# Performance work log

Hardware: AMD Instinct MI355X
Metric: run time of the kernel (lower is better)

The kernel has to match this reference:

```python
import jax, jax.numpy as jnp
import numpy as np

B, N, HIST, PRED, KHOP, H = 64, 1085, 24, 24, 3, 64
FX, FM = 1, 11
F = FX + FM  # node feature dim fed to gnn (12)
E = 17360


def setup_inputs() -> dict:
    key = jax.random.key(0)
    ks = jax.random.split(key, 13)
    s = 0.1
    return {
        "x_hist": jax.random.normal(ks[0], (B, HIST, N, FX), jnp.float32),
        "enc_misc": jax.random.normal(ks[1], (B, HIST, N, FM), jnp.float32),
        "dec": jax.random.normal(ks[2], (B, PRED, N, FM), jnp.float32),
        "We": jax.random.normal(ks[3], (2 * F, F), jnp.float32) * s,
        "be": jnp.zeros((F,), jnp.float32),
        "Wx": jax.random.normal(ks[4], (KHOP, 2 * F, 3 * H), jnp.float32) * s,
        "Wh": jax.random.normal(ks[5], (KHOP, H, 3 * H), jnp.float32) * s,
        "bx": jnp.zeros((KHOP, 3 * H), jnp.float32),
        "bh": jnp.zeros((KHOP, 3 * H), jnp.float32),
        "fc_w": jax.random.normal(ks[6], (KHOP * H, FX), jnp.float32) * s,
        "fc_b": jnp.zeros((FX,), jnp.float32),
        "src": jax.random.randint(ks[7], (E,), 0, N, jnp.int32),
        "dst": jax.random.randint(ks[8], (E,), 0, N, jnp.int32),
    }


def reference(x_hist, enc_misc, dec, We, be, Wx, Wh, bx, bh, fc_w, fc_b, src, dst):
    features = jnp.concatenate([enc_misc, dec], axis=1)  # (B, HIST+PRED, N, FM)

    def gnn(x):  # x: (B, N, F) -> (B, N, F); edge MLP + scatter-sum + residual
        m = jax.nn.relu(jnp.concatenate([x[:, src], x[:, dst]], -1) @ We + be)  # (B,E,F)
        return x + jnp.zeros_like(x).at[:, dst].add(m)

    def gru(x, h, k):  # x: (B*N, 2F), h: (B*N, H)
        g = x @ Wx[k] + bx[k]
        gh = h @ Wh[k] + bh[k]
        r = jax.nn.sigmoid(g[:, :H] + gh[:, :H])
        z = jax.nn.sigmoid(g[:, H:2 * H] + gh[:, H:2 * H])
        n = jnp.tanh(g[:, 2 * H:] + r * gh[:, 2 * H:])
        return (1.0 - z) * n + z * h

    def run_step(hn, xn):  # xn: (B, N, F)
        xg = xn
        new = list(hn)
        for k in range(KHOP):
            xg = gnn(xg)
            x_gru = jnp.concatenate([xg, xn], -1).reshape(B * N, 2 * F)
            new[k] = gru(x_gru, new[k], k)
        return tuple(new)

    h0 = tuple(jnp.zeros((B * N, H), x_hist.dtype) for _ in range(KHOP))

    def hist_step(hn, inp):
        xp, ft = inp  # (B,N,FX), (B,N,FM)
        return run_step(hn, jnp.concatenate([xp, ft], -1)), None

    hist_xs = (jnp.swapaxes(x_hist[:, :HIST - 1], 0, 1),
               jnp.swapaxes(features[:, 1:HIST], 0, 1))
    hn, _ = jax.lax.scan(hist_step, h0, hist_xs)

    def pred_step(carry, ft):
        hn, x = carry
        hn = run_step(hn, jnp.concatenate([x, ft], -1))
        hn_all = jnp.concatenate([h.reshape(B, N, H) for h in hn], -1)  # (B,N,KHOP*H)
        x_new = hn_all @ fc_w + fc_b  # (B, N, FX)
        return (hn, x_new), x_new

    _, ys = jax.lax.scan(pred_step, (hn, x_hist[:, -1]),
                         jnp.swapaxes(features[:, HIST:], 0, 1))
    return jnp.swapaxes(ys, 0, 1)  # (B, PRED, N, FX)
```

## Files before the change

### kernel.cpp

```cpp
#include <hip/hip_runtime.h>

#define NB 64
#define NNODE 1085
#define HIST 24
#define PRED 24
#define KHOP 3
#define HDIM 64
#define FXD 1
#define FMD 11
#define FD 12
#define NE 17360
#define NROWS (NB*NNODE)
#define CHUNK 136

typedef float v4 __attribute__((ext_vector_type(4)));

__device__ __forceinline__ float sigm(float x){ return 1.0f/(1.0f + __expf(-x)); }
__device__ __forceinline__ float tanh_f(float x){ return 1.0f - 2.0f/(__expf(2.0f*x)+1.0f); }

__global__ void csr_count_k(const int* __restrict__ dst, int* __restrict__ deg)
{
    int e = blockIdx.x*256 + threadIdx.x;
    if (e < NE) atomicAdd(&deg[dst[e]], 1);
}

__global__ __launch_bounds__(1024) void csr_scan_k(const int* __restrict__ deg,
                                                   int* __restrict__ offs, int* __restrict__ curs)
{
    __shared__ int s[2][2048];
    int t = threadIdx.x;
    for (int i=t;i<2048;i+=1024) s[0][i] = (i<NNODE) ? deg[i] : 0;
    __syncthreads();
    int cur = 0;
    for (int d=1; d<2048; d<<=1){
        for (int i=t;i<2048;i+=1024){
            int v = s[cur][i];
            if (i>=d) v += s[cur][i-d];
            s[cur^1][i] = v;
        }
        __syncthreads();
        cur ^= 1;
    }
    for (int i=t;i<=NNODE;i+=1024){
        int v = (i==0) ? 0 : s[cur][i-1];
        offs[i] = v;
        if (i<NNODE) curs[i] = v;
    }
}

__global__ void csr_fill_k(const int* __restrict__ dst, int* __restrict__ curs,
                           int* __restrict__ elist)
{
    int e = blockIdx.x*256 + threadIdx.x;
    if (e < NE){
        int d = dst[e];
        int p = atomicAdd(&curs[d], 1);
        elist[p] = e;
    }
}

__global__ void build_hist_k(const float* __restrict__ x_hist, const float* __restrict__ enc_misc,
                             int t0, int T, float* __restrict__ xn_all)
{
    int idx = blockIdx.x*256 + threadIdx.x;
    if (idx >= T*NROWS) return;
    int ti = idx / NROWS, row = idx - ti*NROWS;
    int b = row / NNODE, n = row - b*NNODE;
    int t = t0 + ti;
    float v[12];
    v[0] = x_hist[((long)b*HIST + t)*NNODE + n];
    const float* fp = enc_misc + (((long)b*HIST + (t+1))*NNODE + n)*FMD;
    #pragma unroll
    for (int i=0;i<FMD;i++) v[1+i] = fp[i];
    v4* xp = (v4*)(xn_all + ((long)ti*NROWS + row)*FD);
    #pragma unroll
    for (int q=0;q<3;q++){
        v4 tq; tq[0]=v[4*q]; tq[1]=v[4*q+1]; tq[2]=v[4*q+2]; tq[3]=v[4*q+3];
        xp[q]=tq;
    }
}

__global__ void build_xn_k(const float* __restrict__ xsrc, long xs_bs, long xs_off,
                           const float* __restrict__ feat, long f_bs, long f_off,
                           float* __restrict__ xn)
{
    int row = blockIdx.x*256 + threadIdx.x;
    if (row >= NROWS) return;
    int b = row / NNODE, n = row - b*NNODE;
    float v[12];
    v[0] = xsrc[(long)b*xs_bs + xs_off + n];
    const float* fp = feat + (long)b*f_bs + f_off + (long)n*FMD;
    #pragma unroll
    for (int i=0;i<FMD;i++) v[1+i] = fp[i];
    v4* xp = (v4*)(xn + (long)row*FD);
    #pragma unroll
    for (int q=0;q<3;q++){
        v4 tq; tq[0]=v[4*q]; tq[1]=v[4*q+1]; tq[2]=v[4*q+2]; tq[3]=v[4*q+3];
        xp[q]=tq;
    }
}

__global__ __launch_bounds__(256) void gnn_gather_k(const float* __restrict__ xin,
    const float* __restrict__ We, const float* __restrict__ be,
    const int* __restrict__ src, const int* __restrict__ dst,
    const int* __restrict__ elist, const int* __restrict__ offs,
    float* __restrict__ xout)
{
    __shared__ __align__(16) float x_s[NNODE*FD];
    __shared__ __align__(16) float acc_s[CHUNK*FD];
    __shared__ __align__(16) float w_s[288];
    __shared__ float be_s[12];
    const int t = threadIdx.x;
    const int b = blockIdx.x >> 3, c = blockIdx.x & 7;
    const long ti = blockIdx.y;
    const int n0 = c*CHUNK, n1 = min(NNODE, n0+CHUNK);
    const float* x = xin + ti*NROWS*FD;

    const v4* xg4 = (const v4*)(x + (long)b*NNODE*FD);
    for (int i=t; i<NNODE*FD/4; i+=256) ((v4*)x_s)[i] = xg4[i];
    for (int i=t; i<288; i+=256) w_s[i]=We[i];
    if (t<12) be_s[t]=be[t];
    for (int i=t; i<(n1-n0)*FD; i+=256) acc_s[i]=0.f;
    __syncthreads();

    const int e_beg = offs[n0], e_end = offs[n1];
    const int total = e_end - e_beg;
    const int L = (total + 255) >> 8;
    const int my_beg = e_beg + t*L;
    const int my_end = min(my_beg + L, e_end);

    float accr[12];
    float part[12];
    int cur = -1;

    for (int idx=my_beg; idx<my_end; ++idx){
        int e = elist[idx];
        int sN = src[e], dN = dst[e];
        if (dN != cur){
            if (cur >= 0){
                float* ab = &acc_s[(cur-n0)*FD];
                #pragma unroll
                for (int f=0;f<12;f++) atomicAdd(&ab[f], accr[f]);
            }
            cur = dN;
            #pragma unroll
            for (int f=0;f<12;f++){ accr[f]=0.f; part[f]=be_s[f]; }
            const v4* xdv = (const v4*)&x_s[dN*FD];
            #pragma unroll
            for (int q=0;q<3;q++){
                v4 cc = xdv[q];
                #pragma unroll
                for (int j=0;j<4;j++){
                    float xv = cc[j];
                    int i = (12 + 4*q + j)*12;
                    v4 w0=*(const v4*)&w_s[i];
                    v4 w1=*(const v4*)&w_s[i+4];
                    v4 w2=*(const v4*)&w_s[i+8];
                    #pragma unroll
                    for (int jj=0;jj<4;jj++){
                        part[jj]   += xv*w0[jj];
                        part[4+jj] += xv*w1[jj];
                        part[8+jj] += xv*w2[jj];
                    }
                }
            }
        }
        float m[12];
        #pragma unroll
        for (int f=0;f<12;f++) m[f]=part[f];
        const v4* xsv = (const v4*)&x_s[sN*FD];
        #pragma unroll
        for (int q=0;q<3;q++){
            v4 a = xsv[q];
            #pragma unroll
            for (int j=0;j<4;j++){
                float xv = a[j];
                int i = (4*q + j)*12;
                v4 w0=*(const v4*)&w_s[i];
                v4 w1=*(const v4*)&w_s[i+4];
                v4 w2=*(const v4*)&w_s[i+8];
                #pragma unroll
                for (int jj=0;jj<4;jj++){
                    m[jj]   += xv*w0[jj];
                    m[4+jj] += xv*w1[jj];
                    m[8+jj] += xv*w2[jj];
                }
            }
        }
        #pragma unroll
        for (int f=0;f<12;f++) accr[f] += fmaxf(m[f], 0.f);
    }
    if (cur >= 0){
        float* ab = &acc_s[(cur-n0)*FD];
        #pragma unroll
        for (int f=0;f<12;f++) atomicAdd(&ab[f], accr[f]);
    }
    __syncthreads();

    const int cnt4 = (n1-n0)*FD/4;
    const v4* xs4 = (const v4*)&x_s[n0*FD];
    const v4* ac4 = (const v4*)acc_s;
    v4* ob4 = (v4*)(xout + ti*NROWS*FD + ((long)b*NNODE + n0)*FD);
    for (int i=t; i<cnt4; i+=256) ob4[i] = xs4[i] + ac4[i];
}

#define KC 44
__global__ __launch_bounds__(256) void gru3_k(
    const float* __restrict__ xg_base, long k_stride,
    const float* __restrict__ xn,
    float* __restrict__ h_base,
    const float* __restrict__ Wx, const float* __restrict__ Wh,
    const float* __restrict__ bx, const float* __restrict__ bh)
{
    const int k = blockIdx.y;
    const float* xg  = xg_base + (long)k*k_stride;
    float*       h   = h_base + (size_t)k*NROWS*HDIM;
    const float* wx  = Wx + (size_t)k*24*192;
    const float* wh  = Wh + (size_t)k*64*192;
    const float* bxk = bx + k*192;
    const float* bhk = bh + k*192;

    __shared__ __align__(16) float A_s[KC][64];
    __shared__ __align__(16) float W_s[KC][192];
    const int tid = threadIdx.x;
    const int tx = tid & 15, ty = tid >> 4;
    const long row0 = (long)blockIdx.x * 64;

    const v4* xg4 = (const v4*)(xg + row0*FD);
    const v4* xn4 = (const v4*)(xn + row0*FD);
    const v4* h4  = (const v4*)(h  + row0*HDIM);
    const v4* wx4 = (const v4*)wx;
    const v4* wh4 = (const v4*)wh;

    float acc_r[16], acc_z[16], acc_gn[16], acc_ghn[16];
    #pragma unroll
    for (int i=0;i<16;i++){ acc_r[i]=0.f; acc_z[i]=0.f; acc_gn[i]=0.f; acc_ghn[i]=0.f; }

    for (int i=tid; i<KC*48; i+=256){
        int kk = i/48, q = i - kk*48;
        v4 w = (kk<24) ? wx4[kk*48+q] : wh4[(kk-24)*48+q];
        *(v4*)&W_s[kk][q*4] = w;
    }
    for (int i=tid; i<192; i+=256){
        int r = i/3, q = i - r*3;
        v4 v = xg4[r*3+q];
        #pragma unroll
        for (int j=0;j<4;j++) A_s[4*q+j][r] = v[j];
    }
    for (int i=tid; i<192; i+=256){
        int r = i/3, q = i - r*3;
        v4 v = xn4[r*3+q];
        #pragma unroll
        for (int j=0;j<4;j++) A_s[12+4*q+j][r] = v[j];
    }
    for (int i=tid; i<320; i+=256){
        int r = i/5, q = i - r*5;
        v4 v = h4[r*16+q];
        #pragma unroll
        for (int j=0;j<4;j++) A_s[24+4*q+j][r] = v[j];
    }
    __syncthreads();
    #pragma unroll 4
    for (int kk=0;kk<24;kk++){
        v4 av=*(const v4*)&A_s[kk][ty*4];
        v4 wr=*(const v4*)&W_s[kk][tx*4];
        v4 wz=*(const v4*)&W_s[kk][64+tx*4];
        v4 wn=*(const v4*)&W_s[kk][128+tx*4];
        #pragma unroll
        for (int dr=0;dr<4;dr++)
            #pragma unroll
            for (int dc=0;dc<4;dc++){
                acc_r[dr*4+dc]+=av[dr]*wr[dc];
                acc_z[dr*4+dc]+=av[dr]*wz[dc];
                acc_gn[dr*4+dc]+=av[dr]*wn[dc];
            }
    }
    #pragma unroll 4
    for (int kk=24;kk<44;kk++){
        v4 av=*(const v4*)&A_s[kk][ty*4];
        v4 wr=*(const v4*)&W_s[kk][tx*4];
        v4 wz=*(const v4*)&W_s[kk][64+tx*4];
        v4 wn=*(const v4*)&W_s[kk][128+tx*4];
        #pragma unroll
        for (int dr=0;dr<4;dr++)
            #pragma unroll
            for (int dc=0;dc<4;dc++){
                acc_r[dr*4+dc]+=av[dr]*wr[dc];
                acc_z[dr*4+dc]+=av[dr]*wz[dc];
                acc_ghn[dr*4+dc]+=av[dr]*wn[dc];
            }
    }
    __syncthreads();
    for (int i=tid; i<KC*48; i+=256){
        int kk = i/48, q = i - kk*48;
        *(v4*)&W_s[kk][q*4] = wh4[(20+kk)*48+q];
    }
    for (int i=tid; i<704; i+=256){
        int r = i/11, q = i - r*11;
        v4 v = h4[r*16+5+q];
        #pragma unroll
        for (int j=0;j<4;j++) A_s[4*q+j][r] = v[j];
    }
    __syncthreads();
    #pragma unroll 4
    for (int kk=0;kk<44;kk++){
        v4 av=*(const v4*)&A_s[kk][ty*4];
        v4 wr=*(const v4*)&W_s[kk][tx*4];
        v4 wz=*(const v4*)&W_s[kk][64+tx*4];
        v4 wn=*(const v4*)&W_s[kk][128+tx*4];
        #pragma unroll
        for (int dr=0;dr<4;dr++)
            #pragma unroll
            for (int dc=0;dc<4;dc++){
                acc_r[dr*4+dc]+=av[dr]*wr[dc];
                acc_z[dr*4+dc]+=av[dr]*wz[dc];
                acc_ghn[dr*4+dc]+=av[dr]*wn[dc];
            }
    }

    v4 bxr=*(const v4*)&bxk[tx*4],     bhr=*(const v4*)&bhk[tx*4];
    v4 bxz=*(const v4*)&bxk[64+tx*4],  bhz=*(const v4*)&bhk[64+tx*4];
    v4 bxn=*(const v4*)&bxk[128+tx*4], bhn=*(const v4*)&bhk[128+tx*4];
    #pragma unroll
    for (int dr=0;dr<4;dr++){
        long row = row0 + ty*4 + dr;
        v4 hold = *(const v4*)&h[row*HDIM + tx*4];
        v4 hnew;
        #pragma unroll
        for (int dc=0;dc<4;dc++){
            float rr = sigm(acc_r[dr*4+dc] + bxr[dc] + bhr[dc]);
            float zz = sigm(acc_z[dr*4+dc] + bxz[dc] + bhz[dc]);
            float nn = tanh_f(acc_gn[dr*4+dc] + bxn[dc] + rr*(acc_ghn[dr*4+dc] + bhn[dc]));
            hnew[dc] = (1.0f-zz)*nn + zz*hold[dc];
        }
        *(v4*)&h[row*HDIM + tx*4] = hnew;
    }
}

__global__ void fc_k(const float* __restrict__ h, const float* __restrict__ fc_w,
                     const float* __restrict__ fc_b, float* __restrict__ x_cur,
                     float* __restrict__ out, int p)
{
    int row = blockIdx.x*256+threadIdx.x;
    if (row>=NROWS) return;
    float acc = fc_b[0];
    #pragma unroll
    for (int k=0;k<3;k++){
        const float* hb = h + (long)k*NROWS*HDIM + (long)row*HDIM;
        const float* wb = fc_w + k*HDIM;
        #pragma unroll
        for (int q=0;q<16;q++){
            v4 hv=*(const v4*)&hb[q*4];
            v4 wv=*(const v4*)&wb[q*4];
            acc += hv[0]*wv[0]+hv[1]*wv[1]+hv[2]*wv[2]+hv[3]*wv[3];
        }
    }
    x_cur[row]=acc;
    int b=row/NNODE, n=row-b*NNODE;
    out[((long)b*PRED + p)*NNODE + n] = acc;
}

extern "C" void kernel_launch(void* const* d_in, const int* in_sizes, int n_in,
                              void* d_out, int out_size, void* d_ws, size_t ws_size,
                              hipStream_t stream)
{
    const float* x_hist   = (const float*)d_in[0];
    const float* enc_misc = (const float*)d_in[1];
    const float* dec      = (const float*)d_in[2];
    const float* We       = (const float*)d_in[3];
    const float* be       = (const float*)d_in[4];
    const float* Wx       = (const float*)d_in[5];
    const float* Wh       = (const float*)d_in[6];
    const float* bx       = (const float*)d_in[7];
    const float* bh       = (const float*)d_in[8];
    const float* fc_w     = (const float*)d_in[9];
    const float* fc_b     = (const float*)d_in[10];
    const int*   src      = (const int*)d_in[11];
    const int*   dst      = (const int*)d_in[12];
    float* out = (float*)d_out;

    const size_t SZ_T = (size_t)NROWS*FD;
    size_t fixed_f = (size_t)3*NROWS*HDIM + NROWS + 32*1024;
    size_t avail_f = ws_size/4;
    long tc = 1;
    if (avail_f > fixed_f + 4*SZ_T)
        tc = (long)((avail_f - fixed_f) / (4*SZ_T));
    if (tc > HIST-1) tc = HIST-1;
    if (tc < 1) tc = 1;
    const long T_CHUNK = tc;

    float* h      = (float*)d_ws;
    float* x_cur  = h + (size_t)3*NROWS*HDIM;
    int*   deg    = (int*)(x_cur + NROWS);
    int*   offs   = deg + NNODE;
    int*   curs   = offs + NNODE + 1;
    int*   elist  = curs + NNODE;
    float* xn_all = (float*)(elist + NE) + 16;
    xn_all = (float*)(((size_t)xn_all + 63) & ~(size_t)63);
    float* xg_all = xn_all + T_CHUNK*SZ_T;
    const long K_STRIDE = T_CHUNK*SZ_T;

    hipMemsetAsync(h, 0, (size_t)3*NROWS*HDIM*sizeof(float), stream);
    hipMemsetAsync(deg, 0, NNODE*sizeof(int), stream);

    const int gE = (NE+255)/256;
    csr_count_k<<<gE,256,0,stream>>>(dst, deg);
    csr_scan_k<<<1,1024,0,stream>>>(deg, offs, curs);
    csr_fill_k<<<gE,256,0,stream>>>(dst, curs, elist);

    const int gRow = (NROWS+255)/256;

    for (int t0 = 0; t0 < HIST-1; t0 += (int)T_CHUNK){
        int T = min((int)T_CHUNK, HIST-1-t0);
        build_hist_k<<<(T*NROWS+255)/256,256,0,stream>>>(x_hist, enc_misc, t0, T, xn_all);
        dim3 gG(NB*8, T);
        gnn_gather_k<<<gG,256,0,stream>>>(xn_all,            We,be,src,dst,elist,offs, xg_all);
        gnn_gather_k<<<gG,256,0,stream>>>(xg_all,            We,be,src,dst,elist,offs, xg_all+K_STRIDE);
        gnn_gather_k<<<gG,256,0,stream>>>(xg_all+K_STRIDE,   We,be,src,dst,elist,offs, xg_all+2*K_STRIDE);
        for (int ti=0; ti<T; ti++){
            dim3 gU(NROWS/64, 3);
            gru3_k<<<gU,256,0,stream>>>(xg_all + ti*SZ_T, K_STRIDE,
                                        xn_all + ti*SZ_T, h, Wx, Wh, bx, bh);
        }
    }

    for (int p=0;p<PRED;p++){
        if (p==0)
            build_xn_k<<<gRow,256,0,stream>>>(x_hist,(long)HIST*NNODE,(long)(HIST-1)*NNODE,
                                              dec,(long)PRED*NNODE*FMD,(long)p*NNODE*FMD, xn_all);
        else
            build_xn_k<<<gRow,256,0,stream>>>(x_cur,(long)NNODE,0L,
                                              dec,(long)PRED*NNODE*FMD,(long)p*NNODE*FMD, xn_all);
        dim3 gG(NB*8, 1);
        gnn_gather_k<<<gG,256,0,stream>>>(xn_all,          We,be,src,dst,elist,offs, xg_all);
        gnn_gather_k<<<gG,256,0,stream>>>(xg_all,          We,be,src,dst,elist,offs, xg_all+K_STRIDE);
        gnn_gather_k<<<gG,256,0,stream>>>(xg_all+K_STRIDE, We,be,src,dst,elist,offs, xg_all+2*K_STRIDE);
        dim3 gU(NROWS/64, 3);
        gru3_k<<<gU,256,0,stream>>>(xg_all, K_STRIDE, xn_all, h, Wx, Wh, bx, bh);
        fc_k<<<gRow,256,0,stream>>>(h, fc_w, fc_b, x_cur, out, p);
    }
}
```

Baseline: 12.02 ms.

## Switch to node-major batch-interleaved layout with wave-per-node-range GNN gather

Node feature tensors are stored node-major with the batch index innermost, so each lane of a 64-wide wave handles one batch element of the same node. The GNN gather no longer stages a whole batch graph in LDS. Each wave walks a precomputed, edge-balanced range of destination nodes and reads source features straight from global memory, coalesced across the batch, with no LDS atomics. The CSR stores source indices directly, the GRU blocks load the now-contiguous per-node tiles without a transpose, and the hidden state becomes node-major. This trades LDS reuse of node features for global/L2 gathers and removes the shared-memory occupancy limit and the atomic reductions.

```diff
diff --git a/kernel.cpp b/kernel.cpp
--- a/kernel.cpp
+++ b/kernel.cpp
@@ -11,7 +11,8 @@
 #define FD 12
 #define NE 17360
 #define NROWS (NB*NNODE)
-#define CHUNK 136
+#define WPAR 1024
+
 
 typedef float v4 __attribute__((ext_vector_type(4)));
 
@@ -48,160 +49,116 @@
     }
 }
 
-__global__ void csr_fill_k(const int* __restrict__ dst, int* __restrict__ curs,
-                           int* __restrict__ elist)
+__global__ void csr_fill_k(const int* __restrict__ dst, const int* __restrict__ src,
+                           int* __restrict__ curs, int* __restrict__ esrc)
 {
     int e = blockIdx.x*256 + threadIdx.x;
     if (e < NE){
         int d = dst[e];
         int p = atomicAdd(&curs[d], 1);
-        elist[p] = e;
-    }
+        esrc[p] = src[e];
+    }
+}
+
+__global__ void csr_part_k(const int* __restrict__ offs, int* __restrict__ wpart)
+{
+    int w = blockIdx.x*256 + threadIdx.x;
+    if (w > WPAR) return;
+    if (w == 0)    { wpart[0] = 0;        return; }
+    if (w == WPAR) { wpart[WPAR] = NNODE; return; }
+    int target = (int)(((long)w * NE) / WPAR);
+    int lo = 0, hi = NNODE;
+    while (lo < hi){ int mid = (lo+hi)>>1; if (offs[mid] >= target) hi = mid; else lo = mid+1; }
+    wpart[w] = lo;
 }
 
 __global__ void build_hist_k(const float* __restrict__ x_hist, const float* __restrict__ enc_misc,
                              int t0, int T, float* __restrict__ xn_all)
 {
+    long idx = (long)blockIdx.x*256 + threadIdx.x;
+    if (idx >= (long)T*NROWS) return;
+    int b = (int)(idx & 63);
+    long nn = idx >> 6;
+    int ti = (int)(nn / NNODE);
+    int n  = (int)(nn - (long)ti*NNODE);
+    int t  = t0 + ti;
+    float* xp = xn_all + (long)ti*NROWS*FD + (long)n*FD*64 + b;
+    xp[0] = x_hist[((long)b*HIST + t)*NNODE + n];
+    const float* fp = enc_misc + (((long)b*HIST + (t+1))*NNODE + n)*FMD;
+    #pragma unroll
+    for (int i=0;i<FMD;i++) xp[(1+i)*64] = fp[i];
+}
+
+__global__ void build_xn_k(const float* __restrict__ xsrc, int from_xcur,
+                           const float* __restrict__ dec, int p,
+                           float* __restrict__ xn)
+{
     int idx = blockIdx.x*256 + threadIdx.x;
-    if (idx >= T*NROWS) return;
-    int ti = idx / NROWS, row = idx - ti*NROWS;
-    int b = row / NNODE, n = row - b*NNODE;
-    int t = t0 + ti;
-    float v[12];
-    v[0] = x_hist[((long)b*HIST + t)*NNODE + n];
-    const float* fp = enc_misc + (((long)b*HIST + (t+1))*NNODE + n)*FMD;
-    #pragma unroll
-    for (int i=0;i<FMD;i++) v[1+i] = fp[i];
-    v4* xp = (v4*)(xn_all + ((long)ti*NROWS + row)*FD);
-    #pragma unroll
-    for (int q=0;q<3;q++){
-        v4 tq; tq[0]=v[4*q]; tq[1]=v[4*q+1]; tq[2]=v[4*q+2]; tq[3]=v[4*q+3];
-        xp[q]=tq;
-    }
-}
-
-__global__ void build_xn_k(const float* __restrict__ xsrc, long xs_bs, long xs_off,
-                           const float* __restrict__ feat, long f_bs, long f_off,
-                           float* __restrict__ xn)
-{
-    int row = blockIdx.x*256 + threadIdx.x;
-    if (row >= NROWS) return;
-    int b = row / NNODE, n = row - b*NNODE;
-    float v[12];
-    v[0] = xsrc[(long)b*xs_bs + xs_off + n];
-    const float* fp = feat + (long)b*f_bs + f_off + (long)n*FMD;
-    #pragma unroll
-    for (int i=0;i<FMD;i++) v[1+i] = fp[i];
-    v4* xp = (v4*)(xn + (long)row*FD);
-    #pragma unroll
-    for (int q=0;q<3;q++){
-        v4 tq; tq[0]=v[4*q]; tq[1]=v[4*q+1]; tq[2]=v[4*q+2]; tq[3]=v[4*q+3];
-        xp[q]=tq;
-    }
+    if (idx >= NROWS) return;
+    int b = idx & 63, n = idx >> 6;
+    float v0 = from_xcur ? xsrc[idx]
+                         : xsrc[((long)b*HIST + (HIST-1))*NNODE + n];
+    float* xp = xn + (long)n*FD*64 + b;
+    xp[0] = v0;
+    const float* fp = dec + (((long)b*PRED + p)*NNODE + n)*FMD;
+    #pragma unroll
+    for (int i=0;i<FMD;i++) xp[(1+i)*64] = fp[i];
 }
 
 __global__ __launch_bounds__(256) void gnn_gather_k(const float* __restrict__ xin,
     const float* __restrict__ We, const float* __restrict__ be,
-    const int* __restrict__ src, const int* __restrict__ dst,
-    const int* __restrict__ elist, const int* __restrict__ offs,
-    float* __restrict__ xout)
-{
-    __shared__ __align__(16) float x_s[NNODE*FD];
-    __shared__ __align__(16) float acc_s[CHUNK*FD];
-    __shared__ __align__(16) float w_s[288];
+    const int* __restrict__ esrc, const int* __restrict__ offs,
+    const int* __restrict__ wpart, float* __restrict__ xout)
+{
+    __shared__ float w_s[288];
     __shared__ float be_s[12];
-    const int t = threadIdx.x;
-    const int b = blockIdx.x >> 3, c = blockIdx.x & 7;
-    const long ti = blockIdx.y;
-    const int n0 = c*CHUNK, n1 = min(NNODE, n0+CHUNK);
-    const float* x = xin + ti*NROWS*FD;
-
-    const v4* xg4 = (const v4*)(x + (long)b*NNODE*FD);
-    for (int i=t; i<NNODE*FD/4; i+=256) ((v4*)x_s)[i] = xg4[i];
-    for (int i=t; i<288; i+=256) w_s[i]=We[i];
-    if (t<12) be_s[t]=be[t];
-    for (int i=t; i<(n1-n0)*FD; i+=256) acc_s[i]=0.f;
-    __syncthreads();
-
-    const int e_beg = offs[n0], e_end = offs[n1];
-    const int total = e_end - e_beg;
-    const int L = (total + 255) >> 8;
-    const int my_beg = e_beg + t*L;
-    const int my_end = min(my_beg + L, e_end);
-
-    float accr[12];
-    float part[12];
-    int cur = -1;
-
-    for (int idx=my_beg; idx<my_end; ++idx){
-        int e = elist[idx];
-        int sN = src[e], dN = dst[e];
-        if (dN != cur){
-            if (cur >= 0){
-                float* ab = &acc_s[(cur-n0)*FD];
+    const int tid = threadIdx.x;
+    for (int i=tid;i<288;i+=256) w_s[i]=We[i];
+    if (tid<12) be_s[tid]=be[tid];
+    __syncthreads();
+
+    const int lane = tid & 63;
+    const int wave = (blockIdx.x*256 + tid) >> 6;
+    const long sbase = (long)blockIdx.y * ((long)NROWS*FD);
+    const float* x = xin + sbase;
+    float* xo = xout + sbase;
+
+    const int n0 = wpart[wave], n1 = wpart[wave+1];
+    for (int n=n0; n<n1; ++n){
+        float xd[12], part[12], acc[12];
+        const float* xb = x + (long)n*768 + lane;
+        #pragma unroll
+        for (int f=0;f<12;f++) xd[f] = xb[f*64];
+        #pragma unroll
+        for (int f=0;f<12;f++){ part[f]=be_s[f]; acc[f]=0.f; }
+        #pragma unroll
+        for (int f=0;f<12;f++){
+            float xv = xd[f];
+            const float* wrow = &w_s[(12+f)*12];
+            #pragma unroll
+            for (int j=0;j<12;j++) part[j] += xv*wrow[j];
+        }
+        const int e0 = offs[n], e1 = offs[n+1];
+        for (int idx=e0; idx<e1; ++idx){
+            int s = esrc[idx];
+            const float* xsb = x + (long)s*768 + lane;
+            float m[12];
+            #pragma unroll
+            for (int f=0;f<12;f++) m[f]=part[f];
+            #pragma unroll
+            for (int f=0;f<12;f++){
+                float xv = xsb[f*64];
+                const float* wrow = &w_s[f*12];
                 #pragma unroll
-                for (int f=0;f<12;f++) atomicAdd(&ab[f], accr[f]);
+                for (int j=0;j<12;j++) m[j] += xv*wrow[j];
             }
-            cur = dN;
-            #pragma unroll
-            for (int f=0;f<12;f++){ accr[f]=0.f; part[f]=be_s[f]; }
-            const v4* xdv = (const v4*)&x_s[dN*FD];
-            #pragma unroll
-            for (int q=0;q<3;q++){
-                v4 cc = xdv[q];
-                #pragma unroll
-                for (int j=0;j<4;j++){
-                    float xv = cc[j];
-                    int i = (12 + 4*q + j)*12;
-                    v4 w0=*(const v4*)&w_s[i];
-                    v4 w1=*(const v4*)&w_s[i+4];
-                    v4 w2=*(const v4*)&w_s[i+8];
-                    #pragma unroll
-                    for (int jj=0;jj<4;jj++){
-                        part[jj]   += xv*w0[jj];
-                        part[4+jj] += xv*w1[jj];
-                        part[8+jj] += xv*w2[jj];
-                    }
-                }
-            }
-        }
-        float m[12];
-        #pragma unroll
-        for (int f=0;f<12;f++) m[f]=part[f];
-        const v4* xsv = (const v4*)&x_s[sN*FD];
-        #pragma unroll
-        for (int q=0;q<3;q++){
-            v4 a = xsv[q];
-            #pragma unroll
-            for (int j=0;j<4;j++){
-                float xv = a[j];
-                int i = (4*q + j)*12;
-                v4 w0=*(const v4*)&w_s[i];
-                v4 w1=*(const v4*)&w_s[i+4];
-                v4 w2=*(const v4*)&w_s[i+8];
-                #pragma unroll
-                for (int jj=0;jj<4;jj++){
-                    m[jj]   += xv*w0[jj];
-                    m[4+jj] += xv*w1[jj];
-                    m[8+jj] += xv*w2[jj];
-                }
-            }
-        }
-        #pragma unroll
-        for (int f=0;f<12;f++) accr[f] += fmaxf(m[f], 0.f);
-    }
-    if (cur >= 0){
-        float* ab = &acc_s[(cur-n0)*FD];
-        #pragma unroll
-        for (int f=0;f<12;f++) atomicAdd(&ab[f], accr[f]);
-    }
-    __syncthreads();
-
-    const int cnt4 = (n1-n0)*FD/4;
-    const v4* xs4 = (const v4*)&x_s[n0*FD];
-    const v4* ac4 = (const v4*)acc_s;
-    v4* ob4 = (v4*)(xout + ti*NROWS*FD + ((long)b*NNODE + n0)*FD);
-    for (int i=t; i<cnt4; i+=256) ob4[i] = xs4[i] + ac4[i];
+            #pragma unroll
+            for (int f=0;f<12;f++) acc[f] += fmaxf(m[f],0.f);
+        }
+        float* xob = xo + (long)n*768 + lane;
+        #pragma unroll
+        for (int f=0;f<12;f++) xob[f*64] = xd[f] + acc[f];
+    }
 }
 
 #define KC 44
@@ -213,8 +170,10 @@
     const float* __restrict__ bx, const float* __restrict__ bh)
 {
     const int k = blockIdx.y;
-    const float* xg  = xg_base + (long)k*k_stride;
-    float*       h   = h_base + (size_t)k*NROWS*HDIM;
+    const int n = blockIdx.x;
+    const float* xgn = xg_base + (long)k*k_stride + (long)n*768;
+    const float* xnn = xn + (long)n*768;
+    float*       hn  = h_base + ((size_t)k*NROWS + (long)n*64)*HDIM;
     const float* wx  = Wx + (size_t)k*24*192;
     const float* wh  = Wh + (size_t)k*64*192;
     const float* bxk = bx + k*192;
@@ -224,13 +183,10 @@
     __shared__ __align__(16) float W_s[KC][192];
     const int tid = threadIdx.x;
     const int tx = tid & 15, ty = tid >> 4;
-    const long row0 = (long)blockIdx.x * 64;
-
-    const v4* xg4 = (const v4*)(xg + row0*FD);
-    const v4* xn4 = (const v4*)(xn + row0*FD);
-    const v4* h4  = (const v4*)(h  + row0*HDIM);
+
     const v4* wx4 = (const v4*)wx;
     const v4* wh4 = (const v4*)wh;
+    const v4* h4  = (const v4*)hn;
 
     float acc_r[16], acc_z[16], acc_gn[16], acc_ghn[16];
     #pragma unroll
@@ -241,18 +197,8 @@
         v4 w = (kk<24) ? wx4[kk*48+q] : wh4[(kk-24)*48+q];
         *(v4*)&W_s[kk][q*4] = w;
     }
-    for (int i=tid; i<192; i+=256){
-        int r = i/3, q = i - r*3;
-        v4 v = xg4[r*3+q];
-        #pragma unroll
-        for (int j=0;j<4;j++) A_s[4*q+j][r] = v[j];
-    }
-    for (int i=tid; i<192; i+=256){
-        int r = i/3, q = i - r*3;
-        v4 v = xn4[r*3+q];
-        #pragma unroll
-        for (int j=0;j<4;j++) A_s[12+4*q+j][r] = v[j];
-    }
+    for (int i=tid; i<192; i+=256) ((v4*)A_s)[i]       = ((const v4*)xgn)[i];
+    for (int i=tid; i<192; i+=256) ((v4*)A_s)[192+i]   = ((const v4*)xnn)[i];
     for (int i=tid; i<320; i+=256){
         int r = i/5, q = i - r*5;
         v4 v = h4[r*16+q];
@@ -323,8 +269,8 @@
     v4 bxn=*(const v4*)&bxk[128+tx*4], bhn=*(const v4*)&bhk[128+tx*4];
     #pragma unroll
     for (int dr=0;dr<4;dr++){
-        long row = row0 + ty*4 + dr;
-        v4 hold = *(const v4*)&h[row*HDIM + tx*4];
+        int lr = ty*4 + dr;
+        v4 hold = *(const v4*)&hn[lr*HDIM + tx*4];
         v4 hnew;
         #pragma unroll
         for (int dc=0;dc<4;dc++){
@@ -333,7 +279,7 @@
             float nn = tanh_f(acc_gn[dr*4+dc] + bxn[dc] + rr*(acc_ghn[dr*4+dc] + bhn[dc]));
             hnew[dc] = (1.0f-zz)*nn + zz*hold[dc];
         }
-        *(v4*)&h[row*HDIM + tx*4] = hnew;
+        *(v4*)&hn[lr*HDIM + tx*4] = hnew;
     }
 }
 
@@ -341,12 +287,12 @@
                      const float* __restrict__ fc_b, float* __restrict__ x_cur,
                      float* __restrict__ out, int p)
 {
-    int row = blockIdx.x*256+threadIdx.x;
-    if (row>=NROWS) return;
+    int idx = blockIdx.x*256+threadIdx.x;
+    if (idx>=NROWS) return;
     float acc = fc_b[0];
     #pragma unroll
     for (int k=0;k<3;k++){
-        const float* hb = h + (long)k*NROWS*HDIM + (long)row*HDIM;
+        const float* hb = h + ((size_t)k*NROWS + idx)*HDIM;
         const float* wb = fc_w + k*HDIM;
         #pragma unroll
         for (int q=0;q<16;q++){
@@ -355,8 +301,8 @@
             acc += hv[0]*wv[0]+hv[1]*wv[1]+hv[2]*wv[2]+hv[3]*wv[3];
         }
     }
-    x_cur[row]=acc;
-    int b=row/NNODE, n=row-b*NNODE;
+    x_cur[idx]=acc;
+    int b = idx & 63, n = idx >> 6;
     out[((long)b*PRED + p)*NNODE + n] = acc;
 }
 
@@ -380,7 +326,7 @@
     float* out = (float*)d_out;
 
     const size_t SZ_T = (size_t)NROWS*FD;
-    size_t fixed_f = (size_t)3*NROWS*HDIM + NROWS + 32*1024;
+    size_t fixed_f = (size_t)3*NROWS*HDIM + NROWS + 64*1024;
     size_t avail_f = ws_size/4;
     long tc = 1;
     if (avail_f > fixed_f + 4*SZ_T)
@@ -394,9 +340,10 @@
     int*   deg    = (int*)(x_cur + NROWS);
     int*   offs   = deg + NNODE;
     int*   curs   = offs + NNODE + 1;
-    int*   elist  = curs + NNODE;
-    float* xn_all = (float*)(elist + NE) + 16;
-    xn_all = (float*)(((size_t)xn_all + 63) & ~(size_t)63);
+    int*   wpart  = curs + NNODE;
+    int*   esrc   = wpart + WPAR + 1;
+    float* xn_all = (float*)(esrc + NE) + 16;
+    xn_all = (float*)(((size_t)xn_all + 255) & ~(size_t)255);
     float* xg_all = xn_all + T_CHUNK*SZ_T;
     const long K_STRIDE = T_CHUNK*SZ_T;
 
@@ -406,19 +353,21 @@
     const int gE = (NE+255)/256;
     csr_count_k<<<gE,256,0,stream>>>(dst, deg);
     csr_scan_k<<<1,1024,0,stream>>>(deg, offs, curs);
-    csr_fill_k<<<gE,256,0,stream>>>(dst, curs, elist);
+    csr_fill_k<<<gE,256,0,stream>>>(dst, src, curs, esrc);
+    csr_part_k<<<(WPAR+256)/256,256,0,stream>>>(offs, wpart);
 
     const int gRow = (NROWS+255)/256;
+    const int gGx  = WPAR*64/256;
 
     for (int t0 = 0; t0 < HIST-1; t0 += (int)T_CHUNK){
         int T = min((int)T_CHUNK, HIST-1-t0);
-        build_hist_k<<<(T*NROWS+255)/256,256,0,stream>>>(x_hist, enc_misc, t0, T, xn_all);
-        dim3 gG(NB*8, T);
-        gnn_gather_k<<<gG,256,0,stream>>>(xn_all,            We,be,src,dst,elist,offs, xg_all);
-        gnn_gather_k<<<gG,256,0,stream>>>(xg_all,            We,be,src,dst,elist,offs, xg_all+K_STRIDE);
-        gnn_gather_k<<<gG,256,0,stream>>>(xg_all+K_STRIDE,   We,be,src,dst,elist,offs, xg_all+2*K_STRIDE);
+        build_hist_k<<<(int)(((long)T*NROWS+255)/256),256,0,stream>>>(x_hist, enc_misc, t0, T, xn_all);
+        dim3 gG(gGx, T);
+        gnn_gather_k<<<gG,256,0,stream>>>(xn_all,            We,be,esrc,offs,wpart, xg_all);
+        gnn_gather_k<<<gG,256,0,stream>>>(xg_all,            We,be,esrc,offs,wpart, xg_all+K_STRIDE);
+        gnn_gather_k<<<gG,256,0,stream>>>(xg_all+K_STRIDE,   We,be,esrc,offs,wpart, xg_all+2*K_STRIDE);
         for (int ti=0; ti<T; ti++){
-            dim3 gU(NROWS/64, 3);
+            dim3 gU(NNODE, 3);
             gru3_k<<<gU,256,0,stream>>>(xg_all + ti*SZ_T, K_STRIDE,
                                         xn_all + ti*SZ_T, h, Wx, Wh, bx, bh);
         }
@@ -426,16 +375,14 @@
 
     for (int p=0;p<PRED;p++){
         if (p==0)
-            build_xn_k<<<gRow,256,0,stream>>>(x_hist,(long)HIST*NNODE,(long)(HIST-1)*NNODE,
-                                              dec,(long)PRED*NNODE*FMD,(long)p*NNODE*FMD, xn_all);
+            build_xn_k<<<gRow,256,0,stream>>>(x_hist, 0, dec, p, xn_all);
         else
-            build_xn_k<<<gRow,256,0,stream>>>(x_cur,(long)NNODE,0L,
-                                              dec,(long)PRED*NNODE*FMD,(long)p*NNODE*FMD, xn_all);
-        dim3 gG(NB*8, 1);
-        gnn_gather_k<<<gG,256,0,stream>>>(xn_all,          We,be,src,dst,elist,offs, xg_all);
-        gnn_gather_k<<<gG,256,0,stream>>>(xg_all,          We,be,src,dst,elist,offs, xg_all+K_STRIDE);
-        gnn_gather_k<<<gG,256,0,stream>>>(xg_all+K_STRIDE, We,be,src,dst,elist,offs, xg_all+2*K_STRIDE);
-        dim3 gU(NROWS/64, 3);
+            build_xn_k<<<gRow,256,0,stream>>>(x_cur, 1, dec, p, xn_all);
+        dim3 gG(gGx, 1);
+        gnn_gather_k<<<gG,256,0,stream>>>(xn_all,          We,be,esrc,offs,wpart, xg_all);
+        gnn_gather_k<<<gG,256,0,stream>>>(xg_all,          We,be,esrc,offs,wpart, xg_all+K_STRIDE);
+        gnn_gather_k<<<gG,256,0,stream>>>(xg_all+K_STRIDE, We,be,esrc,offs,wpart, xg_all+2*K_STRIDE);
+        dim3 gU(NNODE, 3);
         gru3_k<<<gU,256,0,stream>>>(xg_all, K_STRIDE, xn_all, h, Wx, Wh, bx, bh);
         fc_k<<<gRow,256,0,stream>>>(h, fc_w, fc_b, x_cur, out, p);
     }
```

After: 13.63 ms. 13.4% more time.
